# Kernel tuning notes

Hardware: AMD Instinct MI355X
Metric: run time of the kernel (lower is better)

The kernel has to match this reference:

```python
import jax, jax.numpy as jnp
import numpy as np

SAMPLE_RATE = 24000.0
HARMONIC_NUM = 8
SINE_AMP = 0.1
DIM = HARMONIC_NUM + 1
BATCH, LENGTH = 16, 480000


def setup_inputs() -> dict:
    key = jax.random.key(0)
    k1, k2, k3 = jax.random.split(key, 3)
    u = jax.random.uniform(k1, (BATCH, LENGTH), dtype=jnp.float32)
    voiced = (jax.random.uniform(k2, (BATCH, LENGTH)) > 0.2).astype(jnp.float32)
    f0 = (80.0 + 400.0 * u) * voiced
    rand_ini = jax.random.uniform(k3, (BATCH, 1, DIM), dtype=jnp.float32)
    return {"f0": f0, "rand_ini": rand_ini}


def reference(f0, rand_ini):
    # f0: [B, L] -> [B, L, 1]
    f0 = f0[..., None]
    harmonics = jnp.arange(1, DIM + 1, dtype=f0.dtype).reshape(1, 1, -1)  # [1,1,DIM]
    rad_values = jnp.mod(f0 * harmonics / SAMPLE_RATE, 1.0)              # [B,L,DIM]
    rad_values = rad_values.at[:, 0:1, :].add(rand_ini)                  # random initial phase
    phase = jnp.cumsum(rad_values, axis=1) * (2.0 * jnp.pi)              # [B,L,DIM]
    uv = (f0 > 0).astype(f0.dtype)                                       # [B,L,1]
    sine_waves = jnp.sin(phase) * SINE_AMP * uv                          # fused scale+mask
    return sine_waves, uv
```

## Files before the change

kernel.cpp:

```cpp
#include <hip/hip_runtime.h>
#include <math.h>

#define BATCH 16
#define LEN 480000
#define NDIM 9
#define CHUNK 1024
#define NCHUNK 469
#define AMP 0.1f

typedef float vfloat4 __attribute__((ext_vector_type(4)));

__device__ __forceinline__ float hw_fract(float x) {
#if __has_builtin(__builtin_amdgcn_fractf)
  return __builtin_amdgcn_fractf(x);
#else
  return x - floorf(x);
#endif
}
__device__ __forceinline__ float hw_sin1(float x) {
#if __has_builtin(__builtin_amdgcn_sinf)
  return __builtin_amdgcn_sinf(x);
#else
  return __sinf(x * 6.283185307179586f);
#endif
}

__global__ __launch_bounds__(256) void sg_partial(const float* __restrict__ f0,
                                                  double* __restrict__ part) {
  const int c = blockIdx.x, b = blockIdx.y, t = threadIdx.x;
  const int i4 = c * 256 + t;
  float4 v = make_float4(0.f, 0.f, 0.f, 0.f);
  if (i4 < LEN / 4) v = ((const float4*)(f0 + (size_t)b * LEN))[i4];
  double s = (double)((v.x + v.y) + (v.z + v.w));
#pragma unroll
  for (int d = 32; d > 0; d >>= 1) s += __shfl_down(s, d, 64);
  __shared__ double ws[4];
  if ((t & 63) == 0) ws[t >> 6] = s;
  __syncthreads();
  if (t == 0) part[(size_t)b * NCHUNK + c] = (ws[0] + ws[1]) + (ws[2] + ws[3]);
}

__global__ __launch_bounds__(256) void sg_main(const float* __restrict__ f0,
                                               const float* __restrict__ rand_ini,
                                               const double* __restrict__ part,
                                               float* __restrict__ out) {
  const int c = blockIdx.x, b = blockIdx.y, t = threadIdx.x;
  const int lane = t & 63, w = t >> 6;

  __shared__ vfloat4 tile[2304];
  __shared__ float wsc[4];
  __shared__ double dred[4];
  __shared__ double cbs_s;

  const int i4 = c * 256 + t;
  float4 v = make_float4(0.f, 0.f, 0.f, 0.f);
  if (i4 < LEN / 4) v = ((const float4*)(f0 + (size_t)b * LEN))[i4];
  const float fvv0 = v.x, fvv1 = v.y, fvv2 = v.z, fvv3 = v.w;
  const float gs = (v.x + v.y) + (v.z + v.w);

  const double* prow = part + (size_t)b * NCHUNK;
  double s = 0.0;
  if (t < c) s += prow[t];
  if (t + 256 < c) s += prow[t + 256];
#pragma unroll
  for (int d = 32; d > 0; d >>= 1) s += __shfl_down(s, d, 64);
  if (lane == 0) dred[w] = s;

  float x = gs;
#pragma unroll
  for (int d = 1; d < 64; d <<= 1) {
    float y = __shfl_up(x, d, 64);
    if (lane >= d) x += y;
  }
  if (lane == 63) wsc[w] = x;
  __syncthreads();
  if (t == 0) cbs_s = (dred[0] + dred[1]) + (dred[2] + dred[3]);
  __syncthreads();

  const float t0 = wsc[0], t1 = wsc[1], t2 = wsc[2];
  const float wpre = (w > 0 ? t0 : 0.f) + (w > 1 ? t1 : 0.f) + (w > 2 ? t2 : 0.f);
  float P = wpre + (x - gs);

  const double cb = cbs_s;
  float phi0[NDIM], hsf[NDIM];
#pragma unroll
  for (int h = 0; h < NDIM; ++h) {
    double hs = (double)(h + 1) * (1.0 / 24000.0);
    double p0 = (double)rand_ini[b * NDIM + h] + hs * cb;
    p0 -= floor(p0);
    phi0[h] = (float)p0;
    hsf[h] = (float)hs;
  }

  float sv[4][NDIM];
  float uvv[4];
  const float fvv[4] = {fvv0, fvv1, fvv2, fvv3};
#pragma unroll
  for (int e = 0; e < 4; ++e) {
    const float f = fvv[e];
    P += f;
    uvv[e] = (f > 0.f) ? 1.f : 0.f;
    const float amp = AMP * uvv[e];
#pragma unroll
    for (int h = 0; h < NDIM; ++h)
      sv[e][h] = amp * hw_sin1(hw_fract(phi0[h] + hsf[h] * P));
  }

#pragma unroll
  for (int j = 0; j < 9; ++j) {
    const int i0 = 4 * j;
    vfloat4 q;
    q.x = sv[(i0    ) / 9][(i0    ) % 9];
    q.y = sv[(i0 + 1) / 9][(i0 + 1) % 9];
    q.z = sv[(i0 + 2) / 9][(i0 + 2) % 9];
    q.w = sv[(i0 + 3) / 9][(i0 + 3) % 9];
    tile[t * 9 + j] = q;
  }
  __syncthreads();

  vfloat4* out4 = (vfloat4*)out;
  const int base = c * CHUNK;
  const int valid = min(CHUNK, LEN - base);
  const int nf4 = (valid * NDIM) >> 2;
  const size_t gb4 = ((size_t)b * LEN * NDIM + (size_t)base * NDIM) >> 2;
#pragma unroll
  for (int k = 0; k < 9; ++k) {
    const int idx = k * 256 + t;
    if (idx < nf4) __builtin_nontemporal_store(tile[idx], &out4[gb4 + idx]);
  }
  const size_t uv4_base = ((size_t)BATCH * LEN * NDIM) / 4 + ((size_t)b * LEN) / 4;
  if (i4 < LEN / 4) {
    vfloat4 u;
    u.x = uvv[0]; u.y = uvv[1]; u.z = uvv[2]; u.w = uvv[3];
    __builtin_nontemporal_store(u, &out4[uv4_base + i4]);
  }
}

extern "C" void kernel_launch(void* const* d_in, const int* in_sizes, int n_in,
                              void* d_out, int out_size, void* d_ws, size_t ws_size,
                              hipStream_t stream) {
  const float* f0 = (const float*)d_in[0];
  const float* rand_ini = (const float*)d_in[1];
  float* out = (float*)d_out;

  double* part = (double*)d_ws;

  dim3 grid(NCHUNK, BATCH);
  sg_partial<<<grid, 256, 0, stream>>>(f0, part);
  sg_main<<<grid, 256, 0, stream>>>(f0, rand_ini, part, out);
}
```

Baseline: 322.6 us.

## Stage prefix phases in LDS and compute sines at output layout positions

Threads no longer compute all 36 sine values for their four samples and then transpose them through a 36 KB LDS tile. Each thread now writes only its four prefix-sum phases and amplitude masks to small LDS arrays. In the store loop it computes the sines for exactly the four output floats it writes, indexing by element and harmonic. This shrinks LDS usage and register pressure and removes the large transpose. The cost is extra index arithmetic, per-element LDS reads of the phase and harmonic tables, and a little redundant work.

```diff
diff --git a/kernel.cpp b/kernel.cpp
--- a/kernel.cpp
+++ b/kernel.cpp
@@ -47,15 +47,15 @@
   const int c = blockIdx.x, b = blockIdx.y, t = threadIdx.x;
   const int lane = t & 63, w = t >> 6;
 
-  __shared__ vfloat4 tile[2304];
+  __shared__ __align__(16) float Pl[CHUNK + 4];
+  __shared__ __align__(16) float Al[CHUNK + 4];
+  __shared__ float2 Hl[NDIM];
   __shared__ float wsc[4];
   __shared__ double dred[4];
-  __shared__ double cbs_s;
 
   const int i4 = c * 256 + t;
   float4 v = make_float4(0.f, 0.f, 0.f, 0.f);
   if (i4 < LEN / 4) v = ((const float4*)(f0 + (size_t)b * LEN))[i4];
-  const float fvv0 = v.x, fvv1 = v.y, fvv2 = v.z, fvv3 = v.w;
   const float gs = (v.x + v.y) + (v.z + v.w);
 
   const double* prow = part + (size_t)b * NCHUNK;
@@ -74,47 +74,32 @@
   }
   if (lane == 63) wsc[w] = x;
   __syncthreads();
-  if (t == 0) cbs_s = (dred[0] + dred[1]) + (dred[2] + dred[3]);
-  __syncthreads();
+
+  if (t < NDIM) {
+    const double cb = (dred[0] + dred[1]) + (dred[2] + dred[3]);
+    const double hs = (double)(t + 1) * (1.0 / 24000.0);
+    double p0 = (double)rand_ini[b * NDIM + t] + hs * cb;
+    p0 -= floor(p0);
+    Hl[t] = make_float2((float)p0, (float)hs);
+  }
 
   const float t0 = wsc[0], t1 = wsc[1], t2 = wsc[2];
   const float wpre = (w > 0 ? t0 : 0.f) + (w > 1 ? t1 : 0.f) + (w > 2 ? t2 : 0.f);
-  float P = wpre + (x - gs);
+  const float Pex = wpre + (x - gs);
 
-  const double cb = cbs_s;
-  float phi0[NDIM], hsf[NDIM];
-#pragma unroll
-  for (int h = 0; h < NDIM; ++h) {
-    double hs = (double)(h + 1) * (1.0 / 24000.0);
-    double p0 = (double)rand_ini[b * NDIM + h] + hs * cb;
-    p0 -= floor(p0);
-    phi0[h] = (float)p0;
-    hsf[h] = (float)hs;
-  }
-
-  float sv[4][NDIM];
-  float uvv[4];
-  const float fvv[4] = {fvv0, fvv1, fvv2, fvv3};
-#pragma unroll
-  for (int e = 0; e < 4; ++e) {
-    const float f = fvv[e];
-    P += f;
-    uvv[e] = (f > 0.f) ? 1.f : 0.f;
-    const float amp = AMP * uvv[e];
-#pragma unroll
-    for (int h = 0; h < NDIM; ++h)
-      sv[e][h] = amp * hw_sin1(hw_fract(phi0[h] + hsf[h] * P));
-  }
-
-#pragma unroll
-  for (int j = 0; j < 9; ++j) {
-    const int i0 = 4 * j;
-    vfloat4 q;
-    q.x = sv[(i0    ) / 9][(i0    ) % 9];
-    q.y = sv[(i0 + 1) / 9][(i0 + 1) % 9];
-    q.z = sv[(i0 + 2) / 9][(i0 + 2) % 9];
-    q.w = sv[(i0 + 3) / 9][(i0 + 3) % 9];
-    tile[t * 9 + j] = q;
+  const float p0v = Pex + v.x;
+  const float p1v = p0v + v.y;
+  const float p2v = p1v + v.z;
+  const float p3v = p2v + v.w;
+  {
+    vfloat4 pq; pq.x = p0v; pq.y = p1v; pq.z = p2v; pq.w = p3v;
+    *(vfloat4*)&Pl[4 * t] = pq;
+    vfloat4 aq;
+    aq.x = (v.x > 0.f) ? AMP : 0.f;
+    aq.y = (v.y > 0.f) ? AMP : 0.f;
+    aq.z = (v.z > 0.f) ? AMP : 0.f;
+    aq.w = (v.w > 0.f) ? AMP : 0.f;
+    *(vfloat4*)&Al[4 * t] = aq;
   }
   __syncthreads();
 
@@ -123,15 +108,46 @@
   const int valid = min(CHUNK, LEN - base);
   const int nf4 = (valid * NDIM) >> 2;
   const size_t gb4 = ((size_t)b * LEN * NDIM + (size_t)base * NDIM) >> 2;
+
+  const int f0i = 4 * t;
+  const int q0 = f0i / 9;
+  const int r0 = f0i % 9;
+
 #pragma unroll
   for (int k = 0; k < 9; ++k) {
     const int idx = k * 256 + t;
-    if (idx < nf4) __builtin_nontemporal_store(tile[idx], &out4[gb4 + idx]);
+    const int K9 = (1024 * k) / 9;
+    const int rk = (1024 * k) % 9;
+    const int rsum = r0 + rk;
+    const int carry = (rsum >= 9) ? 1 : 0;
+    const int e = q0 + K9 + carry;
+    const int r = rsum - 9 * carry;
+    const float PA = Pl[e], PB = Pl[e + 1];
+    const float aA = Al[e], aB = Al[e + 1];
+    float res[4];
+#pragma unroll
+    for (int j = 0; j < 4; ++j) {
+      const int h = r + j;
+      const bool crs = (h >= 9);
+      const int hh = crs ? h - 9 : h;
+      const float2 ph = Hl[hh];
+      const float Pe = crs ? PB : PA;
+      const float am = crs ? aB : aA;
+      res[j] = am * hw_sin1(hw_fract(ph.x + ph.y * Pe));
+    }
+    if (idx < nf4) {
+      vfloat4 q; q.x = res[0]; q.y = res[1]; q.z = res[2]; q.w = res[3];
+      __builtin_nontemporal_store(q, &out4[gb4 + idx]);
+    }
   }
+
   const size_t uv4_base = ((size_t)BATCH * LEN * NDIM) / 4 + ((size_t)b * LEN) / 4;
   if (i4 < LEN / 4) {
     vfloat4 u;
-    u.x = uvv[0]; u.y = uvv[1]; u.z = uvv[2]; u.w = uvv[3];
+    u.x = (v.x > 0.f) ? 1.f : 0.f;
+    u.y = (v.y > 0.f) ? 1.f : 0.f;
+    u.z = (v.z > 0.f) ? 1.f : 0.f;
+    u.w = (v.w > 0.f) ? 1.f : 0.f;
     __builtin_nontemporal_store(u, &out4[uv4_base + i4]);
   }
 }
```

Result: no change. 323.1 us, median of 2 (+0.2%).
